# Optimization experiments

Hardware: AMD Instinct MI355X
Metric: run time of the kernel (lower is better)

The kernel has to match this reference:

```python
import jax, jax.numpy as jnp
import numpy as np

NUM_EDGE_TYPES = 4
TIME_STEPS = (1, 1)  # one propagation step per layer, 2 layers
HIDDEN = 128
N_NODES = 50000
N_EDGES = 400000


def setup_inputs() -> dict:
    key = jax.random.key(0)
    ks = jax.random.split(key, 8)
    states = jax.random.normal(ks[0], (N_NODES, HIDDEN), jnp.float32)
    etype = jax.random.randint(ks[1], (N_EDGES,), 0, NUM_EDGE_TYPES, jnp.int32)
    src = jax.random.randint(ks[2], (N_EDGES,), 0, N_NODES, jnp.int32)
    dst = jax.random.randint(ks[3], (N_EDGES,), 0, N_NODES, jnp.int32)
    edges = jnp.stack([etype, src, dst], axis=-1)  # [E, 3] = (type, src, dst)
    L = len(TIME_STEPS)
    std = HIDDEN ** -0.5  # matches tf.random_normal_initializer(stddev=H**-0.5)
    type_W = jax.random.normal(ks[4], (L, NUM_EDGE_TYPES, HIDDEN, HIDDEN), jnp.float32) * std
    type_b = jax.random.normal(ks[5], (L, NUM_EDGE_TYPES, HIDDEN), jnp.float32) * std
    gru_kernel = jax.random.normal(ks[6], (L, HIDDEN, 3 * HIDDEN), jnp.float32) * std
    gru_rkernel = jax.random.normal(ks[7], (L, HIDDEN, 3 * HIDDEN), jnp.float32) * std
    gru_bias = jnp.zeros((L, 2, 3 * HIDDEN), jnp.float32)  # [input_bias, recurrent_bias]
    return dict(states=states, edges=edges, type_W=type_W, type_b=type_b,
                gru_kernel=gru_kernel, gru_rkernel=gru_rkernel, gru_bias=gru_bias)


def _gru_cell(x, h, kernel, rkernel, bias):
    # tf.keras.layers.GRUCell with defaults (reset_after=True, sigmoid/tanh)
    mx = x @ kernel + bias[0]   # [N, 3H]
    mh = h @ rkernel + bias[1]  # [N, 3H]
    xz, xr, xh = jnp.split(mx, 3, axis=-1)
    hz, hr, hh = jnp.split(mh, 3, axis=-1)
    z = jax.nn.sigmoid(xz + hz)
    r = jax.nn.sigmoid(xr + hr)
    c = jnp.tanh(xh + r * hh)
    return z * h + (1.0 - z) * c


def _propagate(h, layer_no, edges, type_W, type_b):
    etype, src, dst = edges[:, 0], edges[:, 1], edges[:, 2]
    src_states = h[src]  # [E, H] irregular gather
    msgs = jnp.zeros_like(src_states)
    # per-edge-type dense transform, combined via masking (jit-friendly
    # equivalent of tf.dynamic_partition + per-type matmul)
    for t in range(NUM_EDGE_TYPES):
        mt = src_states @ type_W[layer_no, t] + type_b[layer_no, t]
        msgs = msgs + jnp.where((etype == t)[:, None], mt, 0.0)
    # scatter-add messages into destination nodes
    return jax.ops.segment_sum(msgs, dst, num_segments=h.shape[0])


def reference(states, edges, type_W, type_b, gru_kernel, gru_rkernel, gru_bias):
    h = states
    for layer_no, steps in enumerate(TIME_STEPS):
        for _ in range(steps):
            agg = _propagate(h, layer_no, edges, type_W, type_b)
            h = _gru_cell(agg, h, gru_kernel[layer_no], gru_rkernel[layer_no], gru_bias[layer_no])
    return h
```

## Files before the change

kernel.cpp:

```cpp
#include <hip/hip_runtime.h>
#include <hip/hip_bf16.h>

#define H 128
#define NT 4
#define CAP4 40
#define BK 64

typedef __attribute__((ext_vector_type(8))) _Float16 half8;
typedef __attribute__((ext_vector_type(4))) float f32x4;

#if defined(__has_builtin)
#if __has_builtin(__builtin_amdgcn_global_load_lds)
#define HAS_GLL 1
#endif
#endif
#ifndef HAS_GLL
#define HAS_GLL 0
#endif

__device__ __forceinline__ float bf2f(unsigned short u) {
    union { unsigned int i; float f; } v;
    v.i = ((unsigned int)u) << 16;
    return v.f;
}

__device__ __forceinline__ unsigned short f2bf(float f) {
    union { float f; unsigned int i; } v;
    v.f = f;
    unsigned int x = v.i;
    unsigned int r = (x + 0x7fffu + ((x >> 16) & 1u)) >> 16;
    return (unsigned short)r;
}

__device__ __forceinline__ float fsigmoid(float x) {
    return 1.0f / (1.0f + __expf(-x));
}
__device__ __forceinline__ float ftanh(float x) {
    return 1.0f - 2.0f / (__expf(2.0f * x) + 1.0f);
}

__device__ __forceinline__ float readf(const void* p, long i, int isbf) {
    return isbf ? bf2f(((const unsigned short*)p)[i]) : ((const float*)p)[i];
}

__device__ __forceinline__ void gll16(const _Float16* g, _Float16* l) {
#if HAS_GLL
    __builtin_amdgcn_global_load_lds(
        (const __attribute__((address_space(1))) unsigned int*)g,
        (__attribute__((address_space(3))) unsigned int*)l, 16, 0, 0);
#endif
}

__device__ __forceinline__ void stage_tile(
    const _Float16* __restrict__ gbase, int rstride, int row0, int kof,
    int maxrow, _Float16* lds) {
    const int wave = threadIdx.x >> 6, lane = threadIdx.x & 63;
#pragma unroll
    for (int s = 0; s < 4; s++) {
        int R = wave * 32 + s * 8;
        int rl = R + (lane >> 3);
        int rg = row0 + rl;
        if (rg >= maxrow) rg = maxrow - 1;
        int chunk = (lane & 7) ^ (rl & 7);
        const _Float16* gp = gbase + (size_t)rg * rstride + kof + chunk * 8;
#if HAS_GLL
        gll16(gp, lds + R * 64);
#else
        *(half8*)&lds[rl * 64 + (lane & 7) * 8] = *(const half8*)gp;
#endif
    }
}

__device__ __forceinline__ half8 frag(const _Float16* lds, int r, int g) {
    return *(const half8*)&lds[r * 64 + ((g ^ (r & 7)) * 8)];
}

__global__ void detect_dtype(const unsigned short* __restrict__ states_u16,
                             int* __restrict__ flag) {
    __shared__ int cnt;
    if (threadIdx.x == 0) cnt = 0;
    __syncthreads();
    int local = 0;
    for (int i = threadIdx.x; i < 1024; i += 256) {
        unsigned short u = states_u16[2 * i];
        int e = (u >> 7) & 0xFF;
        if (e >= 96 && e <= 158) local++;
    }
    atomicAdd(&cnt, local);
    __syncthreads();
    if (threadIdx.x == 0) *flag = (cnt >= 512) ? 1 : 0;
}

__global__ void cast_h16(const void* __restrict__ in, _Float16* __restrict__ out,
                         const int* __restrict__ flag, int n) {
    int i = blockIdx.x * blockDim.x + threadIdx.x;
    if (i < n) out[i] = (_Float16)readf(in, i, *flag);
}

__global__ void prep_BTw(const void* __restrict__ W, _Float16* __restrict__ BTw,
                         const int* __restrict__ flag, int total) {
    int i = blockIdx.x * 256 + threadIdx.x;
    if (i >= total) return;
    int l = i >> 16;
    int rem = i & 65535;
    int c = rem >> 9, kk = rem & 511;
    int t = kk >> 7, k = kk & 127;
    BTw[i] = (_Float16)readf(W, (((long)(l * NT + t) * H) + k) * H + c, *flag);
}

__global__ void prep_BTg2(const void* __restrict__ gk, const void* __restrict__ gr,
                          _Float16* __restrict__ BTg, const int* __restrict__ flag,
                          int total) {
    int i = blockIdx.x * 256 + threadIdx.x;
    if (i >= total) return;
    int l = i >> 17;
    int rem = i & 131071;
    int nc = rem >> 8, k = rem & 255;
    int g = nc >> 6, gate = (nc >> 4) & 3, m = nc & 15;
    int c = g * 16 + m;
    int fl = *flag;
    float v = 0.0f;
    if (gate == 0) {
        v = (k < 128) ? readf(gk, ((long)l * H + k) * 384 + c, fl)
                      : readf(gr, ((long)l * H + (k - 128)) * 384 + c, fl);
    } else if (gate == 1) {
        v = (k < 128) ? readf(gk, ((long)l * H + k) * 384 + 128 + c, fl)
                      : readf(gr, ((long)l * H + (k - 128)) * 384 + 128 + c, fl);
    } else if (gate == 2) {
        if (k < 128) v = readf(gk, ((long)l * H + k) * 384 + 256 + c, fl);
    } else {
        if (k >= 128) v = readf(gr, ((long)l * H + (k - 128)) * 384 + 256 + c, fl);
    }
    BTg[i] = (_Float16)v;
}

__global__ void prep_bias2(const void* __restrict__ type_b, const void* __restrict__ grub,
                           float* __restrict__ btab, float* __restrict__ gbsum,
                           float* __restrict__ gb0c, float* __restrict__ gb1c,
                           const int* __restrict__ flag, int LAYERS) {
    int i = blockIdx.x * 256 + threadIdx.x;
    int fl = *flag;
    if (i < LAYERS * NT * H) btab[i] = readf(type_b, i, fl);
    if (i < LAYERS * 256) {
        int l = i >> 8, c = i & 255;
        gbsum[i] = readf(grub, (long)l * 768 + c, fl) +
                   readf(grub, (long)l * 768 + 384 + c, fl);
    }
    if (i < LAYERS * H) {
        int l = i >> 7, c = i & 127;
        gb0c[i] = readf(grub, (long)l * 768 + 256 + c, fl);
        gb1c[i] = readf(grub, (long)l * 768 + 384 + 256 + c, fl);
    }
}

__global__ void place_edges4(const int* __restrict__ edges, int* __restrict__ counts4,
                             int* __restrict__ buckets4, int NE) {
    int e = blockIdx.x * 256 + threadIdx.x;
    if (e >= NE) return;
    int t = edges[3 * e], src = edges[3 * e + 1], dst = edges[3 * e + 2];
    int slot = atomicAdd(&counts4[dst * 4 + t], 1);
    if (slot < CAP4) buckets4[((size_t)dst * 4 + t) * CAP4 + slot] = src;
}

__global__ __launch_bounds__(256) void gather4(
    const _Float16* __restrict__ h16, const int* __restrict__ counts4,
    const int* __restrict__ buckets4, _Float16* __restrict__ A4, int NN) {
    int node = blockIdx.x * 4 + (threadIdx.x >> 6);
    int lane = threadIdx.x & 63;
    int q = lane >> 4, i = lane & 15;
    if (node >= NN) return;
    int cnt = counts4[node * 4 + q];
    if (cnt > CAP4) cnt = CAP4;
    const int* bkt = buckets4 + ((size_t)node * 4 + q) * CAP4;

    float acc[8] = {};
    int e = 0;
    for (; e + 2 <= cnt; e += 2) {
        int s0 = bkt[e], s1 = bkt[e + 1];
        half8 v0 = *(const half8*)&h16[(size_t)s0 * H + i * 8];
        half8 v1 = *(const half8*)&h16[(size_t)s1 * H + i * 8];
#pragma unroll
        for (int j = 0; j < 8; j++) acc[j] += (float)v0[j] + (float)v1[j];
    }
    if (e < cnt) {
        int s0 = bkt[e];
        half8 v0 = *(const half8*)&h16[(size_t)s0 * H + i * 8];
#pragma unroll
        for (int j = 0; j < 8; j++) acc[j] += (float)v0[j];
    }

    half8 o;
#pragma unroll
    for (int j = 0; j < 8; j++) o[j] = (_Float16)acc[j];
    *(half8*)&A4[((size_t)node * 4 + q) * H + i * 8] = o;
}

__global__ __launch_bounds__(256) void gemm_agg(
    const _Float16* __restrict__ A4,
    const _Float16* __restrict__ BT,
    _Float16* __restrict__ agg,
    const int4* __restrict__ cnt4, const float* __restrict__ btab,
    int Mrows) {
    __shared__ _Float16 As[128 * 64];
    __shared__ _Float16 Bs[128 * 64];

    const int row0 = blockIdx.x * 128;
    const int tid = threadIdx.x;
    const int wave = tid >> 6, lane = tid & 63;
    const int m = lane & 15, quad = lane >> 4;
    const int wr = (wave & 1) * 64, wc = (wave >> 1) * 64;

    f32x4 acc[4][4] = {};

    for (int kc = 0; kc < 8; kc++) {
        const int k0 = kc * BK;
        __syncthreads();
        stage_tile(A4, 512, row0, k0, Mrows, As);
        stage_tile(BT, 512, 0, k0, 128, Bs);
        __syncthreads();

#pragma unroll
        for (int ks = 0; ks < 2; ks++) {
            half8 a[4], b[4];
#pragma unroll
            for (int mt = 0; mt < 4; mt++)
                a[mt] = frag(As, wr + mt * 16 + m, ks * 4 + quad);
#pragma unroll
            for (int nt = 0; nt < 4; nt++)
                b[nt] = frag(Bs, wc + nt * 16 + m, ks * 4 + quad);
#pragma unroll
            for (int mt = 0; mt < 4; mt++)
#pragma unroll
                for (int nt = 0; nt < 4; nt++)
                    acc[mt][nt] = __builtin_amdgcn_mfma_f32_16x16x32_f16(
                        a[mt], b[nt], acc[mt][nt], 0, 0, 0);
        }
    }

#pragma unroll
    for (int mt = 0; mt < 4; mt++) {
#pragma unroll
        for (int i = 0; i < 4; i++) {
            int row = row0 + wr + mt * 16 + quad * 4 + i;
            if (row >= Mrows) continue;
            int4 c4 = cnt4[row];
#pragma unroll
            for (int nt = 0; nt < 4; nt++) {
                int cl = wc + nt * 16 + m;
                float bias = c4.x * btab[cl] + c4.y * btab[128 + cl] +
                             c4.z * btab[256 + cl] + c4.w * btab[384 + cl];
                agg[(size_t)row * H + cl] = (_Float16)(acc[mt][nt][i] + bias);
            }
        }
    }
}

__global__ __launch_bounds__(256) void gru_gemm_gate(
    const _Float16* __restrict__ agg16,
    const _Float16* __restrict__ h16,
    const _Float16* __restrict__ BT,
    const float* __restrict__ gbsum,
    const float* __restrict__ gb0c,
    const float* __restrict__ gb1c,
    _Float16* __restrict__ hnext,
    void* __restrict__ outbuf,
    const int* __restrict__ flag, int rtiles, int NN) {
    __shared__ _Float16 As[128 * 64];
    __shared__ _Float16 Bs[128 * 64];
    __shared__ _Float16 hg[128 * 32];

    const int b = blockIdx.x;
    const int r_lo = b & 7, y = (b >> 3) & 3, macro = b >> 5;
    const int rt = macro * 8 + r_lo;
    if (rt >= rtiles) return;
    const int row0 = rt * 128;
    const int col0 = y * 128;
    const int tid = threadIdx.x;
    const int wave = tid >> 6, lane = tid & 63;
    const int m = lane & 15, quad = lane >> 4;
    const int wr = (wave & 1) * 64, wc = (wave >> 1) * 64;

    f32x4 acc[4][4] = {};

    for (int kc = 0; kc < 4; kc++) {
        const int k0 = kc * BK;
        __syncthreads();
        if (kc < 2) stage_tile(agg16, H, row0, k0, NN, As);
        else        stage_tile(h16, H, row0, k0 - 128, NN, As);
        stage_tile(BT, 256, col0, k0, 512, Bs);
        if (kc == 0) {
#pragma unroll
            for (int s = 0; s < 2; s++) {
                int idx = s * 256 + tid;
                int r = idx >> 2, cseg = (idx & 3) * 8;
                int rg = row0 + r;
                if (rg >= NN) rg = NN - 1;
                *(half8*)&hg[r * 32 + cseg] =
                    *(const half8*)&h16[(size_t)rg * H + y * 32 + cseg];
            }
        }
        __syncthreads();

#pragma unroll
        for (int ks = 0; ks < 2; ks++) {
            half8 a[4], b8[4];
#pragma unroll
            for (int mt = 0; mt < 4; mt++)
                a[mt] = frag(As, wr + mt * 16 + m, ks * 4 + quad);
#pragma unroll
            for (int nt = 0; nt < 4; nt++)
                b8[nt] = frag(Bs, wc + nt * 16 + m, ks * 4 + quad);
#pragma unroll
            for (int mt = 0; mt < 4; mt++)
#pragma unroll
                for (int nt = 0; nt < 4; nt++)
                    acc[mt][nt] = __builtin_amdgcn_mfma_f32_16x16x32_f16(
                        a[mt], b8[nt], acc[mt][nt], 0, 0, 0);
        }
    }

    const int g = (col0 + wc) >> 6;
    const int c = g * 16 + m;
    const int chg = (wc >> 2) + m;
    const float bz = gbsum[c];
    const float br = gbsum[128 + c];
    const float bx = gb0c[c];
    const float bh = gb1c[c];
    const int fl = outbuf ? *flag : 0;

#pragma unroll
    for (int mt = 0; mt < 4; mt++) {
#pragma unroll
        for (int i = 0; i < 4; i++) {
            int rl = wr + mt * 16 + quad * 4 + i;
            int row = row0 + rl;
            if (row >= NN) continue;
            float z = fsigmoid(acc[mt][0][i] + bz);
            float r = fsigmoid(acc[mt][1][i] + br);
            float cc = ftanh((acc[mt][2][i] + bx) + r * (acc[mt][3][i] + bh));
            float hv = (float)hg[rl * 32 + chg];
            float hn = z * hv + (1.0f - z) * cc;
            size_t oi = (size_t)row * H + c;
            hnext[oi] = (_Float16)hn;
            if (outbuf) {
                if (fl) ((unsigned short*)outbuf)[oi] = f2bf(hn);
                else    ((float*)outbuf)[oi] = hn;
            }
        }
    }
}

extern "C" void kernel_launch(void* const* d_in, const int* in_sizes, int n_in,
                              void* d_out, int out_size, void* d_ws, size_t ws_size,
                              hipStream_t stream) {
    const void* states = d_in[0];
    const int*  edges  = (const int*)d_in[1];
    const void* type_W = d_in[2];
    const void* type_b = d_in[3];
    const void* gruk   = d_in[4];
    const void* grur   = d_in[5];
    const void* grub   = d_in[6];

    const int NN = in_sizes[0] / H;
    const int NE = in_sizes[1] / 3;
    const int nW = in_sizes[2];
    const int LAYERS = nW / (NT * H * H);

    char* w = (char*)d_ws;
    int* flag = (int*)w;                               w += 64;
    _Float16* h16A  = (_Float16*)w;                    w += (size_t)NN * H * 2;
    _Float16* h16B  = (_Float16*)w;                    w += (size_t)NN * H * 2;
    _Float16* agg16 = (_Float16*)w;                    w += (size_t)NN * H * 2;
    _Float16* A4    = (_Float16*)w;                    w += (size_t)NN * 4 * H * 2;
    _Float16* BTw = (_Float16*)w;                      w += (size_t)LAYERS * H * 512 * 2;
    _Float16* BTg = (_Float16*)w;                      w += (size_t)LAYERS * 512 * 256 * 2;
    float* btab  = (float*)w;                          w += (size_t)LAYERS * NT * H * 4;
    float* gbsum = (float*)w;                          w += (size_t)LAYERS * 256 * 4;
    float* gb0c  = (float*)w;                          w += (size_t)LAYERS * H * 4;
    float* gb1c  = (float*)w;                          w += (size_t)LAYERS * H * 4;
    int* counts4 = (int*)w;                            w += (size_t)NN * 4 * 4;
    int* buckets4 = (int*)w;

    detect_dtype<<<1, 256, 0, stream>>>((const unsigned short*)states, flag);

    cast_h16<<<(NN * H + 255) / 256, 256, 0, stream>>>(states, h16A, flag, NN * H);
    prep_BTw<<<(LAYERS * 65536 + 255) / 256, 256, 0, stream>>>(type_W, BTw, flag,
                                                               LAYERS * 65536);
    prep_BTg2<<<(LAYERS * 131072 + 255) / 256, 256, 0, stream>>>(gruk, grur, BTg, flag,
                                                                 LAYERS * 131072);
    prep_bias2<<<4, 256, 0, stream>>>(type_b, grub, btab, gbsum, gb0c, gb1c, flag, LAYERS);

    hipMemsetAsync(counts4, 0, (size_t)NN * 4 * 4, stream);
    place_edges4<<<(NE + 255) / 256, 256, 0, stream>>>(edges, counts4, buckets4, NE);

    const int rtiles = (NN + 127) / 128;
    const int nb_gru = ((rtiles + 7) / 8) * 32;
    for (int L = 0; L < LAYERS; L++) {
        const _Float16* hcur = (L & 1) ? h16B : h16A;
        _Float16* hnext      = (L & 1) ? h16A : h16B;

        gather4<<<(NN + 3) / 4, 256, 0, stream>>>(hcur, counts4, buckets4, A4, NN);

        gemm_agg<<<rtiles, 256, 0, stream>>>(
            A4, BTw + (size_t)L * H * 512, agg16,
            (const int4*)counts4, btab + (size_t)L * NT * H, NN);

        gru_gemm_gate<<<nb_gru, 256, 0, stream>>>(
            agg16, hcur,
            BTg + (size_t)L * 512 * 256,
            gbsum + (size_t)L * 256, gb0c + (size_t)L * H, gb1c + (size_t)L * H,
            hnext, (L == LAYERS - 1) ? d_out : nullptr, flag, rtiles, NN);
    }
}
```

Baseline: 300.1 us.

## Fuse per-type neighbor gather into aggregation GEMM and skip unused GRU gate MFMAs

Per-type neighbor sums are now computed directly into the shared-memory A tile inside the aggregation GEMM, with 64-row tiles. This removes the separate gather kernel and the round trip of the NN x 512 fp16 A4 intermediate through global memory. The GRU gate GEMM also issues only three of its four column MFMA tiles per K chunk, skipping the input-side or recurrent-side block whose output is not needed. The cost is that each thread walks its edge lists serially inside the GEMM loop, which adds latency between barriers and may lower MFMA utilisation.

```diff
diff --git a/kernel.cpp b/kernel.cpp
--- a/kernel.cpp
+++ b/kernel.cpp
@@ -162,90 +162,90 @@
     if (slot < CAP4) buckets4[((size_t)dst * 4 + t) * CAP4 + slot] = src;
 }
 
-__global__ __launch_bounds__(256) void gather4(
-    const _Float16* __restrict__ h16, const int* __restrict__ counts4,
-    const int* __restrict__ buckets4, _Float16* __restrict__ A4, int NN) {
-    int node = blockIdx.x * 4 + (threadIdx.x >> 6);
-    int lane = threadIdx.x & 63;
-    int q = lane >> 4, i = lane & 15;
-    if (node >= NN) return;
-    int cnt = counts4[node * 4 + q];
-    if (cnt > CAP4) cnt = CAP4;
-    const int* bkt = buckets4 + ((size_t)node * 4 + q) * CAP4;
-
-    float acc[8] = {};
-    int e = 0;
-    for (; e + 2 <= cnt; e += 2) {
-        int s0 = bkt[e], s1 = bkt[e + 1];
-        half8 v0 = *(const half8*)&h16[(size_t)s0 * H + i * 8];
-        half8 v1 = *(const half8*)&h16[(size_t)s1 * H + i * 8];
-#pragma unroll
-        for (int j = 0; j < 8; j++) acc[j] += (float)v0[j] + (float)v1[j];
-    }
-    if (e < cnt) {
-        int s0 = bkt[e];
-        half8 v0 = *(const half8*)&h16[(size_t)s0 * H + i * 8];
-#pragma unroll
-        for (int j = 0; j < 8; j++) acc[j] += (float)v0[j];
-    }
-
-    half8 o;
-#pragma unroll
-    for (int j = 0; j < 8; j++) o[j] = (_Float16)acc[j];
-    *(half8*)&A4[((size_t)node * 4 + q) * H + i * 8] = o;
-}
-
-__global__ __launch_bounds__(256) void gemm_agg(
-    const _Float16* __restrict__ A4,
+__global__ __launch_bounds__(256) void gather_gemm_agg(
+    const _Float16* __restrict__ h16,
+    const int* __restrict__ counts4,
+    const int* __restrict__ buckets4,
     const _Float16* __restrict__ BT,
+    const float* __restrict__ btab,
     _Float16* __restrict__ agg,
-    const int4* __restrict__ cnt4, const float* __restrict__ btab,
     int Mrows) {
-    __shared__ _Float16 As[128 * 64];
+    __shared__ _Float16 As[64 * 64];
     __shared__ _Float16 Bs[128 * 64];
 
-    const int row0 = blockIdx.x * 128;
+    const int row0 = blockIdx.x * 64;
     const int tid = threadIdx.x;
     const int wave = tid >> 6, lane = tid & 63;
     const int m = lane & 15, quad = lane >> 4;
-    const int wr = (wave & 1) * 64, wc = (wave >> 1) * 64;
-
-    f32x4 acc[4][4] = {};
+    const int wc = wave * 32;
+
+    const int gr = tid >> 2, part = tid & 3;
+    int grow = row0 + gr;
+    if (grow >= Mrows) grow = Mrows - 1;
+
+    f32x4 acc[4][2] = {};
 
     for (int kc = 0; kc < 8; kc++) {
-        const int k0 = kc * BK;
+        const int t = kc >> 1, hf = kc & 1;
         __syncthreads();
-        stage_tile(A4, 512, row0, k0, Mrows, As);
-        stage_tile(BT, 512, 0, k0, 128, Bs);
+        stage_tile(BT, 512, 0, kc * BK, 128, Bs);
+
+        {
+            int cnt = counts4[grow * 4 + t];
+            if (cnt > CAP4) cnt = CAP4;
+            const int* bkt = buckets4 + ((size_t)grow * 4 + t) * CAP4;
+            float a[16] = {};
+            for (int e = 0; e < cnt; e++) {
+                const _Float16* hp =
+                    &h16[(size_t)bkt[e] * H + hf * 64 + part * 16];
+                half8 v0 = *(const half8*)hp;
+                half8 v1 = *(const half8*)(hp + 8);
+#pragma unroll
+                for (int j = 0; j < 8; j++) {
+                    a[j] += (float)v0[j];
+                    a[8 + j] += (float)v1[j];
+                }
+            }
+            half8 o0, o1;
+#pragma unroll
+            for (int j = 0; j < 8; j++) {
+                o0[j] = (_Float16)a[j];
+                o1[j] = (_Float16)a[8 + j];
+            }
+            const int p0 = part * 2;
+            *(half8*)&As[gr * 64 + ((p0 ^ (gr & 7)) * 8)] = o0;
+            *(half8*)&As[gr * 64 + (((p0 + 1) ^ (gr & 7)) * 8)] = o1;
+        }
         __syncthreads();
 
 #pragma unroll
         for (int ks = 0; ks < 2; ks++) {
-            half8 a[4], b[4];
+            half8 a[4], b[2];
 #pragma unroll
             for (int mt = 0; mt < 4; mt++)
-                a[mt] = frag(As, wr + mt * 16 + m, ks * 4 + quad);
-#pragma unroll
-            for (int nt = 0; nt < 4; nt++)
+                a[mt] = frag(As, mt * 16 + m, ks * 4 + quad);
+#pragma unroll
+            for (int nt = 0; nt < 2; nt++)
                 b[nt] = frag(Bs, wc + nt * 16 + m, ks * 4 + quad);
 #pragma unroll
             for (int mt = 0; mt < 4; mt++)
 #pragma unroll
-                for (int nt = 0; nt < 4; nt++)
+                for (int nt = 0; nt < 2; nt++)
                     acc[mt][nt] = __builtin_amdgcn_mfma_f32_16x16x32_f16(
                         a[mt], b[nt], acc[mt][nt], 0, 0, 0);
         }
     }
 
+    const int4* cnt4 = (const int4*)counts4;
 #pragma unroll
     for (int mt = 0; mt < 4; mt++) {
 #pragma unroll
         for (int i = 0; i < 4; i++) {
-            int row = row0 + wr + mt * 16 + quad * 4 + i;
+            int row = row0 + mt * 16 + quad * 4 + i;
             if (row >= Mrows) continue;
             int4 c4 = cnt4[row];
 #pragma unroll
-            for (int nt = 0; nt < 4; nt++) {
+            for (int nt = 0; nt < 2; nt++) {
                 int cl = wc + nt * 16 + m;
                 float bias = c4.x * btab[cl] + c4.y * btab[128 + cl] +
                              c4.z * btab[256 + cl] + c4.w * btab[384 + cl];
@@ -284,6 +284,7 @@
 
     for (int kc = 0; kc < 4; kc++) {
         const int k0 = kc * BK;
+        const int ntA = (kc < 2) ? 2 : 3;
         __syncthreads();
         if (kc < 2) stage_tile(agg16, H, row0, k0, NN, As);
         else        stage_tile(h16, H, row0, k0 - 128, NN, As);
@@ -303,19 +304,22 @@
 
 #pragma unroll
         for (int ks = 0; ks < 2; ks++) {
-            half8 a[4], b8[4];
+            half8 a[4], b8[3];
 #pragma unroll
             for (int mt = 0; mt < 4; mt++)
                 a[mt] = frag(As, wr + mt * 16 + m, ks * 4 + quad);
-#pragma unroll
-            for (int nt = 0; nt < 4; nt++)
-                b8[nt] = frag(Bs, wc + nt * 16 + m, ks * 4 + quad);
-#pragma unroll
-            for (int mt = 0; mt < 4; mt++)
-#pragma unroll
-                for (int nt = 0; nt < 4; nt++)
-                    acc[mt][nt] = __builtin_amdgcn_mfma_f32_16x16x32_f16(
-                        a[mt], b8[nt], acc[mt][nt], 0, 0, 0);
+            b8[0] = frag(Bs, wc + 0 * 16 + m, ks * 4 + quad);
+            b8[1] = frag(Bs, wc + 1 * 16 + m, ks * 4 + quad);
+            b8[2] = frag(Bs, wc + ntA * 16 + m, ks * 4 + quad);
+#pragma unroll
+            for (int mt = 0; mt < 4; mt++) {
+                acc[mt][0] = __builtin_amdgcn_mfma_f32_16x16x32_f16(
+                    a[mt], b8[0], acc[mt][0], 0, 0, 0);
+                acc[mt][1] = __builtin_amdgcn_mfma_f32_16x16x32_f16(
+                    a[mt], b8[1], acc[mt][1], 0, 0, 0);
+                acc[mt][ntA] = __builtin_amdgcn_mfma_f32_16x16x32_f16(
+                    a[mt], b8[2], acc[mt][ntA], 0, 0, 0);
+            }
         }
     }
 
@@ -371,7 +375,6 @@
     _Float16* h16A  = (_Float16*)w;                    w += (size_t)NN * H * 2;
     _Float16* h16B  = (_Float16*)w;                    w += (size_t)NN * H * 2;
     _Float16* agg16 = (_Float16*)w;                    w += (size_t)NN * H * 2;
-    _Float16* A4    = (_Float16*)w;                    w += (size_t)NN * 4 * H * 2;
     _Float16* BTw = (_Float16*)w;                      w += (size_t)LAYERS * H * 512 * 2;
     _Float16* BTg = (_Float16*)w;                      w += (size_t)LAYERS * 512 * 256 * 2;
     float* btab  = (float*)w;                          w += (size_t)LAYERS * NT * H * 4;
@@ -394,16 +397,16 @@
     place_edges4<<<(NE + 255) / 256, 256, 0, stream>>>(edges, counts4, buckets4, NE);
 
     const int rtiles = (NN + 127) / 128;
+    const int atiles = (NN + 63) / 64;
     const int nb_gru = ((rtiles + 7) / 8) * 32;
     for (int L = 0; L < LAYERS; L++) {
         const _Float16* hcur = (L & 1) ? h16B : h16A;
         _Float16* hnext      = (L & 1) ? h16A : h16B;
 
-        gather4<<<(NN + 3) / 4, 256, 0, stream>>>(hcur, counts4, buckets4, A4, NN);
-
-        gemm_agg<<<rtiles, 256, 0, stream>>>(
-            A4, BTw + (size_t)L * H * 512, agg16,
-            (const int4*)counts4, btab + (size_t)L * NT * H, NN);
+        gather_gemm_agg<<<atiles, 256, 0, stream>>>(
+            hcur, counts4, buckets4,
+            BTw + (size_t)L * H * 512, btab + (size_t)L * NT * H,
+            agg16, NN);
 
         gru_gemm_gate<<<nb_gru, 256, 0, stream>>>(
             agg16, hcur,
```

After: 303.2 us. Within noise of the previous version (+1.0%).

## Merge preprocessing kernels into one launch and skip zero-block GRU MFMAs

Applied to the files above, without the earlier changes.

Folds the state cast, weight transposes, bias prep and the counts memset into a single prep_all kernel, cutting several launches and one memset from the preprocessing phase. In the GRU gate GEMM, each wave now issues MFMAs for only three of its four 16-column groups per K chunk, since the packed weight layout has zero blocks for the candidate gate (input half only in one group, recurrent half only in the other). This removes a quarter of the MFMA work and B-fragment loads, at the cost of relying on that exact packing layout for correctness.

```diff
diff --git a/kernel.cpp b/kernel.cpp
--- a/kernel.cpp
+++ b/kernel.cpp
@@ -91,65 +91,72 @@
     if (threadIdx.x == 0) *flag = (cnt >= 512) ? 1 : 0;
 }
 
-__global__ void cast_h16(const void* __restrict__ in, _Float16* __restrict__ out,
-                         const int* __restrict__ flag, int n) {
-    int i = blockIdx.x * blockDim.x + threadIdx.x;
-    if (i < n) out[i] = (_Float16)readf(in, i, *flag);
-}
-
-__global__ void prep_BTw(const void* __restrict__ W, _Float16* __restrict__ BTw,
-                         const int* __restrict__ flag, int total) {
-    int i = blockIdx.x * 256 + threadIdx.x;
-    if (i >= total) return;
-    int l = i >> 16;
-    int rem = i & 65535;
-    int c = rem >> 9, kk = rem & 511;
-    int t = kk >> 7, k = kk & 127;
-    BTw[i] = (_Float16)readf(W, (((long)(l * NT + t) * H) + k) * H + c, *flag);
-}
-
-__global__ void prep_BTg2(const void* __restrict__ gk, const void* __restrict__ gr,
-                          _Float16* __restrict__ BTg, const int* __restrict__ flag,
-                          int total) {
-    int i = blockIdx.x * 256 + threadIdx.x;
-    if (i >= total) return;
-    int l = i >> 17;
-    int rem = i & 131071;
-    int nc = rem >> 8, k = rem & 255;
-    int g = nc >> 6, gate = (nc >> 4) & 3, m = nc & 15;
-    int c = g * 16 + m;
-    int fl = *flag;
-    float v = 0.0f;
-    if (gate == 0) {
-        v = (k < 128) ? readf(gk, ((long)l * H + k) * 384 + c, fl)
-                      : readf(gr, ((long)l * H + (k - 128)) * 384 + c, fl);
-    } else if (gate == 1) {
-        v = (k < 128) ? readf(gk, ((long)l * H + k) * 384 + 128 + c, fl)
-                      : readf(gr, ((long)l * H + (k - 128)) * 384 + 128 + c, fl);
-    } else if (gate == 2) {
-        if (k < 128) v = readf(gk, ((long)l * H + k) * 384 + 256 + c, fl);
-    } else {
-        if (k >= 128) v = readf(gr, ((long)l * H + (k - 128)) * 384 + 256 + c, fl);
-    }
-    BTg[i] = (_Float16)v;
-}
-
-__global__ void prep_bias2(const void* __restrict__ type_b, const void* __restrict__ grub,
-                           float* __restrict__ btab, float* __restrict__ gbsum,
-                           float* __restrict__ gb0c, float* __restrict__ gb1c,
-                           const int* __restrict__ flag, int LAYERS) {
-    int i = blockIdx.x * 256 + threadIdx.x;
-    int fl = *flag;
-    if (i < LAYERS * NT * H) btab[i] = readf(type_b, i, fl);
-    if (i < LAYERS * 256) {
-        int l = i >> 8, c = i & 255;
-        gbsum[i] = readf(grub, (long)l * 768 + c, fl) +
-                   readf(grub, (long)l * 768 + 384 + c, fl);
-    }
-    if (i < LAYERS * H) {
-        int l = i >> 7, c = i & 127;
-        gb0c[i] = readf(grub, (long)l * 768 + 256 + c, fl);
-        gb1c[i] = readf(grub, (long)l * 768 + 384 + 256 + c, fl);
+__global__ void prep_all(
+    const void* __restrict__ states, const void* __restrict__ type_W,
+    const void* __restrict__ type_b, const void* __restrict__ gk,
+    const void* __restrict__ gr, const void* __restrict__ grub,
+    _Float16* __restrict__ h16, _Float16* __restrict__ BTw,
+    _Float16* __restrict__ BTg, float* __restrict__ btab,
+    float* __restrict__ gbsum, float* __restrict__ gb0c,
+    float* __restrict__ gb1c, int* __restrict__ counts4,
+    const int* __restrict__ flag,
+    long NNH, int nBTw, int nBTg, int NC4, int LAYERS) {
+    long i = (long)blockIdx.x * 256 + threadIdx.x;
+    const int fl = *flag;
+    if (i < NNH) {
+        h16[i] = (_Float16)readf(states, i, fl);
+        return;
+    }
+    i -= NNH;
+    if (i < nBTw) {
+        int l = (int)(i >> 16);
+        int rem = (int)(i & 65535);
+        int c = rem >> 9, kk = rem & 511;
+        int t = kk >> 7, k = kk & 127;
+        BTw[i] = (_Float16)readf(type_W, (((long)(l * NT + t) * H) + k) * H + c, fl);
+        return;
+    }
+    i -= nBTw;
+    if (i < nBTg) {
+        int l = (int)(i >> 17);
+        int rem = (int)(i & 131071);
+        int nc = rem >> 8, k = rem & 255;
+        int g = nc >> 6, gate = (nc >> 4) & 3, m = nc & 15;
+        int c = g * 16 + m;
+        float v = 0.0f;
+        if (gate == 0) {
+            v = (k < 128) ? readf(gk, ((long)l * H + k) * 384 + c, fl)
+                          : readf(gr, ((long)l * H + (k - 128)) * 384 + c, fl);
+        } else if (gate == 1) {
+            v = (k < 128) ? readf(gk, ((long)l * H + k) * 384 + 128 + c, fl)
+                          : readf(gr, ((long)l * H + (k - 128)) * 384 + 128 + c, fl);
+        } else if (gate == 2) {
+            if (k < 128) v = readf(gk, ((long)l * H + k) * 384 + 256 + c, fl);
+        } else {
+            if (k >= 128) v = readf(gr, ((long)l * H + (k - 128)) * 384 + 256 + c, fl);
+        }
+        BTg[i] = (_Float16)v;
+        return;
+    }
+    i -= nBTg;
+    if (i < NC4) {
+        counts4[i] = 0;
+        return;
+    }
+    i -= NC4;
+    {
+        int j = (int)i;
+        if (j < LAYERS * NT * H) btab[j] = readf(type_b, j, fl);
+        if (j < LAYERS * 256) {
+            int l = j >> 8, c = j & 255;
+            gbsum[j] = readf(grub, (long)l * 768 + c, fl) +
+                       readf(grub, (long)l * 768 + 384 + c, fl);
+        }
+        if (j < LAYERS * H) {
+            int l = j >> 7, c = j & 127;
+            gb0c[j] = readf(grub, (long)l * 768 + 256 + c, fl);
+            gb1c[j] = readf(grub, (long)l * 768 + 384 + 256 + c, fl);
+        }
     }
 }
 
@@ -284,6 +291,7 @@
 
     for (int kc = 0; kc < 4; kc++) {
         const int k0 = kc * BK;
+        const int ntA = (kc < 2) ? 2 : 3;
         __syncthreads();
         if (kc < 2) stage_tile(agg16, H, row0, k0, NN, As);
         else        stage_tile(h16, H, row0, k0 - 128, NN, As);
@@ -303,19 +311,22 @@
 
 #pragma unroll
         for (int ks = 0; ks < 2; ks++) {
-            half8 a[4], b8[4];
+            half8 a[4], b8[3];
 #pragma unroll
             for (int mt = 0; mt < 4; mt++)
                 a[mt] = frag(As, wr + mt * 16 + m, ks * 4 + quad);
-#pragma unroll
-            for (int nt = 0; nt < 4; nt++)
-                b8[nt] = frag(Bs, wc + nt * 16 + m, ks * 4 + quad);
-#pragma unroll
-            for (int mt = 0; mt < 4; mt++)
-#pragma unroll
-                for (int nt = 0; nt < 4; nt++)
-                    acc[mt][nt] = __builtin_amdgcn_mfma_f32_16x16x32_f16(
-                        a[mt], b8[nt], acc[mt][nt], 0, 0, 0);
+            b8[0] = frag(Bs, wc + 0 * 16 + m, ks * 4 + quad);
+            b8[1] = frag(Bs, wc + 1 * 16 + m, ks * 4 + quad);
+            b8[2] = frag(Bs, wc + ntA * 16 + m, ks * 4 + quad);
+#pragma unroll
+            for (int mt = 0; mt < 4; mt++) {
+                acc[mt][0] = __builtin_amdgcn_mfma_f32_16x16x32_f16(
+                    a[mt], b8[0], acc[mt][0], 0, 0, 0);
+                acc[mt][1] = __builtin_amdgcn_mfma_f32_16x16x32_f16(
+                    a[mt], b8[1], acc[mt][1], 0, 0, 0);
+                acc[mt][ntA] = __builtin_amdgcn_mfma_f32_16x16x32_f16(
+                    a[mt], b8[2], acc[mt][ntA], 0, 0, 0);
+            }
         }
     }
 
@@ -383,14 +394,16 @@
 
     detect_dtype<<<1, 256, 0, stream>>>((const unsigned short*)states, flag);
 
-    cast_h16<<<(NN * H + 255) / 256, 256, 0, stream>>>(states, h16A, flag, NN * H);
-    prep_BTw<<<(LAYERS * 65536 + 255) / 256, 256, 0, stream>>>(type_W, BTw, flag,
-                                                               LAYERS * 65536);
-    prep_BTg2<<<(LAYERS * 131072 + 255) / 256, 256, 0, stream>>>(gruk, grur, BTg, flag,
-                                                                 LAYERS * 131072);
-    prep_bias2<<<4, 256, 0, stream>>>(type_b, grub, btab, gbsum, gb0c, gb1c, flag, LAYERS);
-
-    hipMemsetAsync(counts4, 0, (size_t)NN * 4 * 4, stream);
+    const long NNH = (long)NN * H;
+    const int nBTw = LAYERS * 65536;
+    const int nBTg = LAYERS * 131072;
+    const int NC4 = NN * 4;
+    const long ptotal = NNH + nBTw + nBTg + NC4 + LAYERS * NT * H;
+    prep_all<<<(int)((ptotal + 255) / 256), 256, 0, stream>>>(
+        states, type_W, type_b, gruk, grur, grub,
+        h16A, BTw, BTg, btab, gbsum, gb0c, gb1c, counts4, flag,
+        NNH, nBTw, nBTg, NC4, LAYERS);
+
     place_edges4<<<(NE + 255) / 256, 256, 0, stream>>>(edges, counts4, buckets4, NE);
 
     const int rtiles = (NN + 127) / 128;
```

Result: faster. 290.2 us (-3.3%).
